# Kernel tuning notes

Hardware: AMD Instinct MI355X
Metric: run time of the kernel (lower is better)

## Reference

```python
import jax, jax.numpy as jnp
import numpy as np

VOCAB, EMB, HID = 128, 8, 32
B, T = 512, 512


def setup_inputs() -> dict:
    key = jax.random.key(0)
    ks = jax.random.split(key, 8)
    s_emb = 1.0  # torch nn.Embedding init: N(0,1)
    s_lstm = 1.0 / np.sqrt(HID)  # torch LSTM init: U(-1/sqrt(H), 1/sqrt(H))
    s_lin = 1.0 / np.sqrt(HID)
    return {
        "tokens": jax.random.randint(ks[0], (B, T), 0, VOCAB),
        "emb": jax.random.normal(ks[1], (VOCAB, EMB), jnp.float32) * s_emb,
        "w_ih": jax.random.uniform(ks[2], (4 * HID, EMB), jnp.float32, -s_lstm, s_lstm),
        "w_hh": jax.random.uniform(ks[3], (4 * HID, HID), jnp.float32, -s_lstm, s_lstm),
        "b_ih": jax.random.uniform(ks[4], (4 * HID,), jnp.float32, -s_lstm, s_lstm),
        "b_hh": jax.random.uniform(ks[5], (4 * HID,), jnp.float32, -s_lstm, s_lstm),
        "w_out": jax.random.uniform(ks[6], (VOCAB, HID), jnp.float32, -s_lin, s_lin),
        "b_out": jax.random.uniform(ks[7], (VOCAB,), jnp.float32, -s_lin, s_lin),
    }


def _lstm(x_bte, w_ih, w_hh, b_ih, b_hh):
    # x_bte: [B, T, E] -> hidden states [B, T, H]. PyTorch gate order: i, f, g, o.
    b = b_ih + b_hh
    # Precompute input projection for all timesteps: [B, T, 4H]
    x_proj = jnp.einsum("bte,ge->btg", x_bte, w_ih) + b
    x_proj_t = jnp.swapaxes(x_proj, 0, 1)  # [T, B, 4H]
    h0 = jnp.zeros((x_bte.shape[0], HID), x_bte.dtype)
    c0 = jnp.zeros_like(h0)

    def step(carry, xp):
        h, c = carry
        gates = xp + h @ w_hh.T  # [B, 4H]
        i, f, g, o = jnp.split(gates, 4, axis=-1)
        c = jax.nn.sigmoid(f) * c + jax.nn.sigmoid(i) * jnp.tanh(g)
        h = jax.nn.sigmoid(o) * jnp.tanh(c)
        return (h, c), h

    _, h_all = jax.lax.scan(step, (h0, c0), x_proj_t)  # [T, B, H]
    return jnp.swapaxes(h_all, 0, 1)  # [B, T, H]


def reference(tokens, emb, w_ih, w_hh, b_ih, b_hh, w_out, b_out):
    x = emb[tokens]  # [B, T, E] embedding lookup
    h = _lstm(x, w_ih, w_hh, b_ih, b_hh)  # [B, T, H]
    return h @ w_out.T + b_out  # [B, T, VOCAB]
```

## Files before the change

kernel.cpp:

```cpp
#include <hip/hip_runtime.h>

#define VOCAB 128
#define EMB   8
#define HID   32
#define BATCH 512
#define SEQ   512
#define G4    128
#define KB    8

#define LOG2E 1.4426950408889634f

typedef float v2f __attribute__((ext_vector_type(2)));

__global__ void build_proj(const float* __restrict__ emb,
                           const float* __restrict__ w_ih,
                           const float* __restrict__ b_ih,
                           const float* __restrict__ b_hh,
                           float* __restrict__ proj) {
    int idx = blockIdx.x * blockDim.x + threadIdx.x;
    int v = idx >> 7;
    int r = idx & 127;
    float acc = b_ih[r] + b_hh[r];
#pragma unroll
    for (int e = 0; e < EMB; ++e)
        acc += emb[v * EMB + e] * w_ih[r * EMB + e];
    float sc = (r >= 64 && r < 96) ? (2.0f * LOG2E) : LOG2E;
    proj[v * G4 + r] = acc * sc;
}

__device__ __forceinline__ float sig2(float x) {
    return __builtin_amdgcn_rcpf(1.0f + __builtin_amdgcn_exp2f(-x));
}
__device__ __forceinline__ float tanh2(float x2) {
    return 1.0f - 2.0f * __builtin_amdgcn_rcpf(__builtin_amdgcn_exp2f(x2) + 1.0f);
}

__device__ __forceinline__ void half_bcast(float acc, float& lo, float& hi) {
    asm("v_mov_b32 %0, %2\n\t"
        "v_mov_b32 %1, %2\n\t"
        "v_permlane32_swap_b32 %0, %1"
        : "=&v"(lo), "=&v"(hi)
        : "v"(acc));
}

__global__ __launch_bounds__(64)
__attribute__((amdgpu_waves_per_eu(1, 1)))
void lstm_rec(
    const int*   __restrict__ tokens,
    const float* __restrict__ w_hh,
    const float* __restrict__ proj,
    float*       __restrict__ h_out)
{
    const int b    = blockIdx.x;
    const int lane = threadIdx.x;

    __shared__ float sproj[VOCAB * G4];

    {
        const float4* src = (const float4*)proj;
        float4*       dst = (float4*)sproj;
#pragma unroll 4
        for (int i = 0; i < (VOCAB * G4 / 4) / 64; ++i)
            dst[i * 64 + lane] = src[i * 64 + lane];
    }

    const float sc1 = (lane < 32) ? (2.0f * LOG2E) : LOG2E;
    v2f w0p[HID / 2], w1p[HID / 2];
#pragma unroll
    for (int p = 0; p < HID / 2; ++p) {
        w0p[p][0] = w_hh[lane * HID + 2 * p]     * LOG2E;
        w0p[p][1] = w_hh[lane * HID + 2 * p + 1] * LOG2E;
        w1p[p][0] = w_hh[(lane + 64) * HID + 2 * p]     * sc1;
        w1p[p][1] = w_hh[(lane + 64) * HID + 2 * p + 1] * sc1;
    }
#pragma unroll
    for (int p = 0; p < HID / 2; ++p) {
        asm volatile("" : "+v"(w0p[p]), "+v"(w1p[p]));
    }

    const int* tok = tokens + b * SEQ;
    int tv[KB];
    {
        int4 a = ((const int4*)tok)[lane * 2];
        int4 d = ((const int4*)tok)[lane * 2 + 1];
        tv[0] = a.x; tv[1] = a.y; tv[2] = a.z; tv[3] = a.w;
        tv[4] = d.x; tv[5] = d.y; tv[6] = d.z; tv[7] = d.w;
    }

    __syncthreads();

    float h = 0.0f, c = 0.0f;
    float* hp = h_out + (size_t)b * SEQ * HID + lane;
    float hsave[KB];

    float xc0[KB], xc1[KB];

#pragma unroll
    for (int k = 0; k < KB; ++k) {
        int tk = __builtin_amdgcn_readlane(tv[k], 0);
        xc0[k] = sproj[tk * G4 + lane];
        xc1[k] = sproj[tk * G4 + 64 + lane];
    }

    for (int t0 = 0; t0 < SEQ; t0 += KB) {
        const int nb = t0 + KB;
        const int ln = (nb < SEQ) ? (nb >> 3) : 0;
        float xn0[KB], xn1[KB];
#pragma unroll
        for (int k = 0; k < KB; ++k) {
            int tk = __builtin_amdgcn_readlane(tv[k], ln);
            xn0[k] = sproj[tk * G4 + lane];
            xn1[k] = sproj[tk * G4 + 64 + lane];
        }
        __builtin_amdgcn_sched_barrier(0);

#pragma unroll
        for (int k = 0; k < KB; ++k) {
            unsigned hb = __float_as_uint(h);
            v2f hup[HID / 2];
#pragma unroll
            for (int p = 0; p < HID / 2; ++p) {
                hup[p][0] = __uint_as_float(__builtin_amdgcn_readlane(hb, 2 * p));
                hup[p][1] = __uint_as_float(__builtin_amdgcn_readlane(hb, 2 * p + 1));
            }
            __builtin_amdgcn_sched_barrier(0);

            v2f sA = {xc0[k], 0.0f}, sB = {0.0f, 0.0f},
                sC = {0.0f, 0.0f},   sD = {0.0f, 0.0f};
            v2f uA = {xc1[k], 0.0f}, uB = {0.0f, 0.0f},
                uC = {0.0f, 0.0f},   uD = {0.0f, 0.0f};
#pragma unroll
            for (int p = 0; p < HID / 2; p += 4) {
                sA = __builtin_elementwise_fma(hup[p],     w0p[p],     sA);
                sB = __builtin_elementwise_fma(hup[p + 1], w0p[p + 1], sB);
                sC = __builtin_elementwise_fma(hup[p + 2], w0p[p + 2], sC);
                sD = __builtin_elementwise_fma(hup[p + 3], w0p[p + 3], sD);
                uA = __builtin_elementwise_fma(hup[p],     w1p[p],     uA);
                uB = __builtin_elementwise_fma(hup[p + 1], w1p[p + 1], uB);
                uC = __builtin_elementwise_fma(hup[p + 2], w1p[p + 2], uC);
                uD = __builtin_elementwise_fma(hup[p + 3], w1p[p + 3], uD);
            }
            v2f sS = (sA + sB) + (sC + sD);
            v2f uS = (uA + uB) + (uC + uD);
            float acc0 = sS[0] + sS[1];
            float acc1 = uS[0] + uS[1];

            float iv, fv, gv, ov;
            half_bcast(acc0, iv, fv);
            half_bcast(acc1, gv, ov);

            c = sig2(fv) * c + sig2(iv) * tanh2(gv);
            h = sig2(ov) * tanh2(c * (2.0f * LOG2E));

            hsave[k] = h;
        }

        if (lane < 32) {
#pragma unroll
            for (int k = 0; k < KB; ++k)
                hp[(size_t)(t0 + k) * HID] = hsave[k];
        }

#pragma unroll
        for (int k = 0; k < KB; ++k) {
            xc0[k] = xn0[k];
            xc1[k] = xn1[k];
        }
    }
}

#define POS_PER_WAVE 16

__global__ __launch_bounds__(256) void out_proj(
    const float* __restrict__ h,
    const float* __restrict__ w_out,
    const float* __restrict__ b_out,
    float*       __restrict__ out)
{
    const int gtid = blockIdx.x * blockDim.x + threadIdx.x;
    const int wave = gtid >> 6;
    const int lane = threadIdx.x & 63;

    float wv0[HID], wv1[HID];
#pragma unroll
    for (int j = 0; j < HID; ++j) {
        wv0[j] = w_out[lane * HID + j];
        wv1[j] = w_out[(lane + 64) * HID + j];
    }
    const float bb0 = b_out[lane];
    const float bb1 = b_out[lane + 64];

    int pos0 = wave * POS_PER_WAVE;
    for (int p = 0; p < POS_PER_WAVE; ++p) {
        int pos = __builtin_amdgcn_readfirstlane(pos0 + p);
        const float* hp = h + (size_t)pos * HID;
        float a0 = bb0, a1 = bb1;
#pragma unroll
        for (int j4 = 0; j4 < HID / 4; ++j4) {
            float4 hv = *reinterpret_cast<const float4*>(hp + 4 * j4);
            a0 = fmaf(hv.x, wv0[4 * j4 + 0], a0);
            a1 = fmaf(hv.x, wv1[4 * j4 + 0], a1);
            a0 = fmaf(hv.y, wv0[4 * j4 + 1], a0);
            a1 = fmaf(hv.y, wv1[4 * j4 + 1], a1);
            a0 = fmaf(hv.z, wv0[4 * j4 + 2], a0);
            a1 = fmaf(hv.z, wv1[4 * j4 + 2], a1);
            a0 = fmaf(hv.w, wv0[4 * j4 + 3], a0);
            a1 = fmaf(hv.w, wv1[4 * j4 + 3], a1);
        }
        out[(size_t)pos * VOCAB + lane]      = a0;
        out[(size_t)pos * VOCAB + 64 + lane] = a1;
    }
}

extern "C" void kernel_launch(void* const* d_in, const int* in_sizes, int n_in,
                              void* d_out, int out_size, void* d_ws, size_t ws_size,
                              hipStream_t stream) {
    const int*   tokens = (const int*)  d_in[0];
    const float* emb    = (const float*)d_in[1];
    const float* w_ih   = (const float*)d_in[2];
    const float* w_hh   = (const float*)d_in[3];
    const float* b_ih   = (const float*)d_in[4];
    const float* b_hh   = (const float*)d_in[5];
    const float* w_out  = (const float*)d_in[6];
    const float* b_out  = (const float*)d_in[7];
    float*       out    = (float*)d_out;

    float* proj = (float*)d_ws;
    float* hbuf = (float*)((char*)d_ws + VOCAB * G4 * sizeof(float));

    build_proj<<<(VOCAB * G4) / 256, 256, 0, stream>>>(emb, w_ih, b_ih, b_hh, proj);

    lstm_rec<<<BATCH, 64, 0, stream>>>(tokens, w_hh, proj, hbuf);

    const int total_pos = BATCH * SEQ;
    const int waves     = total_pos / POS_PER_WAVE;
    out_proj<<<waves / 4, 256, 0, stream>>>(hbuf, w_out, b_out, out);
}
```

Baseline: 186.9 us.

## Fuse output projection into LSTM recurrence kernel, dropping hidden-state buffer

Each recurrence step now also computes the vocab logits for the previous timestep from the already-broadcast hidden vector. It does this with w_out held in registers, and the last timestep is handled after the loop. This removes the separate out_proj kernel and the write and re-read of the intermediate hidden-state buffer. In exchange it adds about 32 packed FMAs per step inside the serial recurrence, more register use, and the large output stores now come from only 512 single-wave blocks.

```diff
diff --git a/kernel.cpp b/kernel.cpp
--- a/kernel.cpp
+++ b/kernel.cpp
@@ -45,11 +45,13 @@
 
 __global__ __launch_bounds__(64)
 __attribute__((amdgpu_waves_per_eu(1, 1)))
-void lstm_rec(
+void lstm_fused(
     const int*   __restrict__ tokens,
     const float* __restrict__ w_hh,
     const float* __restrict__ proj,
-    float*       __restrict__ h_out)
+    const float* __restrict__ w_out,
+    const float* __restrict__ b_out,
+    float*       __restrict__ out)
 {
     const int b    = blockIdx.x;
     const int lane = threadIdx.x;
@@ -77,6 +79,21 @@
     for (int p = 0; p < HID / 2; ++p) {
         asm volatile("" : "+v"(w0p[p]), "+v"(w1p[p]));
     }
+
+    v2f wop0[HID / 2], wop1[HID / 2];
+#pragma unroll
+    for (int p = 0; p < HID / 2; ++p) {
+        wop0[p][0] = w_out[lane * HID + 2 * p];
+        wop0[p][1] = w_out[lane * HID + 2 * p + 1];
+        wop1[p][0] = w_out[(lane + 64) * HID + 2 * p];
+        wop1[p][1] = w_out[(lane + 64) * HID + 2 * p + 1];
+    }
+#pragma unroll
+    for (int p = 0; p < HID / 2; ++p) {
+        asm volatile("" : "+v"(wop0[p]), "+v"(wop1[p]));
+    }
+    const float bb0 = b_out[lane];
+    const float bb1 = b_out[lane + 64];
 
     const int* tok = tokens + b * SEQ;
     int tv[KB];
@@ -90,11 +107,10 @@
     __syncthreads();
 
     float h = 0.0f, c = 0.0f;
-    float* hp = h_out + (size_t)b * SEQ * HID + lane;
-    float hsave[KB];
+    float* op = out + (size_t)b * SEQ * VOCAB;
+    float lsave0[KB], lsave1[KB];
 
     float xc0[KB], xc1[KB];
-
 #pragma unroll
     for (int k = 0; k < KB; ++k) {
         int tk = __builtin_amdgcn_readlane(tv[k], 0);
@@ -124,6 +140,28 @@
                 hup[p][1] = __uint_as_float(__builtin_amdgcn_readlane(hb, 2 * p + 1));
             }
             __builtin_amdgcn_sched_barrier(0);
+
+            {
+                v2f lA = {0.0f, 0.0f}, lB = {0.0f, 0.0f},
+                    lC = {0.0f, 0.0f}, lD = {0.0f, 0.0f};
+                v2f mA = {0.0f, 0.0f}, mB = {0.0f, 0.0f},
+                    mC = {0.0f, 0.0f}, mD = {0.0f, 0.0f};
+#pragma unroll
+                for (int p = 0; p < HID / 2; p += 4) {
+                    lA = __builtin_elementwise_fma(hup[p],     wop0[p],     lA);
+                    lB = __builtin_elementwise_fma(hup[p + 1], wop0[p + 1], lB);
+                    lC = __builtin_elementwise_fma(hup[p + 2], wop0[p + 2], lC);
+                    lD = __builtin_elementwise_fma(hup[p + 3], wop0[p + 3], lD);
+                    mA = __builtin_elementwise_fma(hup[p],     wop1[p],     mA);
+                    mB = __builtin_elementwise_fma(hup[p + 1], wop1[p + 1], mB);
+                    mC = __builtin_elementwise_fma(hup[p + 2], wop1[p + 2], mC);
+                    mD = __builtin_elementwise_fma(hup[p + 3], wop1[p + 3], mD);
+                }
+                v2f lS = (lA + lB) + (lC + lD);
+                v2f mS = (mA + mB) + (mC + mD);
+                lsave0[k] = lS[0] + lS[1] + bb0;
+                lsave1[k] = mS[0] + mS[1] + bb1;
+            }
 
             v2f sA = {xc0[k], 0.0f}, sB = {0.0f, 0.0f},
                 sC = {0.0f, 0.0f},   sD = {0.0f, 0.0f};
@@ -152,13 +190,16 @@
             c = sig2(fv) * c + sig2(iv) * tanh2(gv);
             h = sig2(ov) * tanh2(c * (2.0f * LOG2E));
 
-            hsave[k] = h;
-        }
-
-        if (lane < 32) {
-#pragma unroll
-            for (int k = 0; k < KB; ++k)
-                hp[(size_t)(t0 + k) * HID] = hsave[k];
+            xc0[k] = 0.0f;
+        }
+
+#pragma unroll
+        for (int k = 0; k < KB; ++k) {
+            const int p = t0 + k - 1;
+            if (p >= 0) {
+                op[(size_t)p * VOCAB + lane]      = lsave0[k];
+                op[(size_t)p * VOCAB + 64 + lane] = lsave1[k];
+            }
         }
 
 #pragma unroll
@@ -167,48 +208,34 @@
             xc1[k] = xn1[k];
         }
     }
-}
-
-#define POS_PER_WAVE 16
-
-__global__ __launch_bounds__(256) void out_proj(
-    const float* __restrict__ h,
-    const float* __restrict__ w_out,
-    const float* __restrict__ b_out,
-    float*       __restrict__ out)
-{
-    const int gtid = blockIdx.x * blockDim.x + threadIdx.x;
-    const int wave = gtid >> 6;
-    const int lane = threadIdx.x & 63;
-
-    float wv0[HID], wv1[HID];
-#pragma unroll
-    for (int j = 0; j < HID; ++j) {
-        wv0[j] = w_out[lane * HID + j];
-        wv1[j] = w_out[(lane + 64) * HID + j];
-    }
-    const float bb0 = b_out[lane];
-    const float bb1 = b_out[lane + 64];
-
-    int pos0 = wave * POS_PER_WAVE;
-    for (int p = 0; p < POS_PER_WAVE; ++p) {
-        int pos = __builtin_amdgcn_readfirstlane(pos0 + p);
-        const float* hp = h + (size_t)pos * HID;
-        float a0 = bb0, a1 = bb1;
-#pragma unroll
-        for (int j4 = 0; j4 < HID / 4; ++j4) {
-            float4 hv = *reinterpret_cast<const float4*>(hp + 4 * j4);
-            a0 = fmaf(hv.x, wv0[4 * j4 + 0], a0);
-            a1 = fmaf(hv.x, wv1[4 * j4 + 0], a1);
-            a0 = fmaf(hv.y, wv0[4 * j4 + 1], a0);
-            a1 = fmaf(hv.y, wv1[4 * j4 + 1], a1);
-            a0 = fmaf(hv.z, wv0[4 * j4 + 2], a0);
-            a1 = fmaf(hv.z, wv1[4 * j4 + 2], a1);
-            a0 = fmaf(hv.w, wv0[4 * j4 + 3], a0);
-            a1 = fmaf(hv.w, wv1[4 * j4 + 3], a1);
-        }
-        out[(size_t)pos * VOCAB + lane]      = a0;
-        out[(size_t)pos * VOCAB + 64 + lane] = a1;
+
+    {
+        unsigned hb = __float_as_uint(h);
+        v2f hup[HID / 2];
+#pragma unroll
+        for (int p = 0; p < HID / 2; ++p) {
+            hup[p][0] = __uint_as_float(__builtin_amdgcn_readlane(hb, 2 * p));
+            hup[p][1] = __uint_as_float(__builtin_amdgcn_readlane(hb, 2 * p + 1));
+        }
+        v2f lA = {0.0f, 0.0f}, lB = {0.0f, 0.0f},
+            lC = {0.0f, 0.0f}, lD = {0.0f, 0.0f};
+        v2f mA = {0.0f, 0.0f}, mB = {0.0f, 0.0f},
+            mC = {0.0f, 0.0f}, mD = {0.0f, 0.0f};
+#pragma unroll
+        for (int p = 0; p < HID / 2; p += 4) {
+            lA = __builtin_elementwise_fma(hup[p],     wop0[p],     lA);
+            lB = __builtin_elementwise_fma(hup[p + 1], wop0[p + 1], lB);
+            lC = __builtin_elementwise_fma(hup[p + 2], wop0[p + 2], lC);
+            lD = __builtin_elementwise_fma(hup[p + 3], wop0[p + 3], lD);
+            mA = __builtin_elementwise_fma(hup[p],     wop1[p],     mA);
+            mB = __builtin_elementwise_fma(hup[p + 1], wop1[p + 1], mB);
+            mC = __builtin_elementwise_fma(hup[p + 2], wop1[p + 2], mC);
+            mD = __builtin_elementwise_fma(hup[p + 3], wop1[p + 3], mD);
+        }
+        v2f lS = (lA + lB) + (lC + lD);
+        v2f mS = (mA + mB) + (mC + mD);
+        op[(size_t)(SEQ - 1) * VOCAB + lane]      = lS[0] + lS[1] + bb0;
+        op[(size_t)(SEQ - 1) * VOCAB + 64 + lane] = mS[0] + mS[1] + bb1;
     }
 }
 
@@ -226,13 +253,8 @@
     float*       out    = (float*)d_out;
 
     float* proj = (float*)d_ws;
-    float* hbuf = (float*)((char*)d_ws + VOCAB * G4 * sizeof(float));
 
     build_proj<<<(VOCAB * G4) / 256, 256, 0, stream>>>(emb, w_ih, b_ih, b_hh, proj);
 
-    lstm_rec<<<BATCH, 64, 0, stream>>>(tokens, w_hh, proj, hbuf);
-
-    const int total_pos = BATCH * SEQ;
-    const int waves     = total_pos / POS_PER_WAVE;
-    out_proj<<<waves / 4, 256, 0, stream>>>(hbuf, w_out, b_out, out);
-}
+    lstm_fused<<<BATCH, 64, 0, stream>>>(tokens, w_hh, proj, w_out, b_out, out);
+}
```

New measurement: 221.7 us. 1.19x slower.
